# Kernel optimization log

Measured on AMD Instinct MI355X. Metric: run time of the kernel, lower is better.

## Reference

```python
import jax, jax.numpy as jnp
import numpy as np

N = 100000
E = 1600000
D_IN = 128
D_OUT = 128
NEG_SLOPE = 0.01  # PyTorch LeakyReLU default


def setup_inputs() -> dict:
    key = jax.random.key(0)
    ks = jax.random.split(key, 6)
    x = jax.random.normal(ks[0], (N, D_IN), dtype=jnp.float32)
    src = jax.random.randint(ks[1], (E,), 0, N, dtype=jnp.int32)
    dst = jax.random.randint(ks[2], (E,), 0, N, dtype=jnp.int32)
    e_attn = jax.random.uniform(ks[3], (E,), dtype=jnp.float32)
    # Xavier-normal-ish init for linear weights
    std = float(np.sqrt(2.0 / (D_IN + D_OUT)))
    W1 = jax.random.normal(ks[4], (D_OUT, D_IN), dtype=jnp.float32) * std
    W2 = jax.random.normal(ks[5], (D_OUT, D_IN), dtype=jnp.float32) * std
    b1 = jnp.zeros((D_OUT,), dtype=jnp.float32)
    b2 = jnp.zeros((D_OUT,), dtype=jnp.float32)
    return {"x": x, "src": src, "dst": dst, "e_attn": e_attn,
            "W1": W1, "b1": b1, "W2": W2, "b2": b2}


def leaky_relu(v):
    return jnp.where(v >= 0, v, NEG_SLOPE * v)


def reference(x, src, dst, e_attn, W1, b1, W2, b2):
    # Edge-weighted gather-scatter: h_n[d] = sum_{e: dst(e)=d} a_e * x[src(e)]
    msgs = x[src] * e_attn[:, None]                      # [E, D_IN]
    h_n = jax.ops.segment_sum(msgs, dst, num_segments=N)  # [N, D_IN]
    # Bi-interaction: LeakyReLU(W1(x + h_n)) + LeakyReLU(W2(x * h_n))
    add_part = leaky_relu(jnp.einsum('nd,od->no', x + h_n, W1) + b1)
    mul_part = leaky_relu(jnp.einsum('nd,od->no', x * h_n, W2) + b2)
    return add_part + mul_part  # dropout p=0.0 -> identity
```

## Files before the change

kernel.cpp:

```cpp
#include <hip/hip_runtime.h>

#define N_NODES 100000
#define E_EDGES 1600000
#define D 128
#define AP 132
#define ASTR 136

typedef short s16x8 __attribute__((ext_vector_type(8)));
typedef unsigned short u16x8 __attribute__((ext_vector_type(8)));
typedef float f32x4 __attribute__((ext_vector_type(4)));

__device__ __forceinline__ unsigned short f2bf(float f) {
    union { float f; unsigned u; } v;
    v.f = f;
    unsigned r = v.u + 0x7FFFu + ((v.u >> 16) & 1u);
    return (unsigned short)(r >> 16);
}

__device__ __forceinline__ float bf2f(unsigned short u) {
    union { unsigned u; float f; } v;
    v.u = ((unsigned)u) << 16;
    return v.f;
}

__device__ __forceinline__ float lrelu(float v) {
    return v >= 0.0f ? v : 0.01f * v;
}

__global__ __launch_bounds__(256) void prep_kernel(
    const int* __restrict__ dst, int* __restrict__ cnt,
    unsigned char* __restrict__ rank, int stride,
    const float* __restrict__ x, unsigned short* __restrict__ xbf, int do_xconv,
    const float* __restrict__ W1, const float* __restrict__ W2,
    unsigned short* __restrict__ Wswz) {
    int b = blockIdx.x;
    int t = threadIdx.x;
    if (b < 6250) {
        int e = b * 256 + t;
        rank[e] = (unsigned char)atomicAdd(&cnt[(size_t)dst[e] * stride], 1);
    } else if (b < 12500) {
        if (!do_xconv) return;
        int idx = (b - 6250) * 256 + t;
        const float4* xp = (const float4*)(x) + (size_t)idx * 2;
        float4 a = xp[0], bb = xp[1];
        u16x8 o;
        o[0] = f2bf(a.x);  o[1] = f2bf(a.y);  o[2] = f2bf(a.z);  o[3] = f2bf(a.w);
        o[4] = f2bf(bb.x); o[5] = f2bf(bb.y); o[6] = f2bf(bb.z); o[7] = f2bf(bb.w);
        ((u16x8*)(xbf))[idx] = o;
    } else {
        int tid = (b - 12500) * 256 + t;
        if (tid >= 2 * 4 * 8 * 64) return;
        int lane = tid & 63;
        int ct   = (tid >> 6) & 7;
        int ks   = (tid >> 9) & 3;
        int mat  = tid >> 11;
        const float* W = mat ? W2 : W1;
        int o  = ct * 16 + (lane & 15);
        int k0 = ks * 32 + (lane >> 4) * 8;
        const float* sp = W + (size_t)o * D + k0;
        u16x8 w;
#pragma unroll
        for (int j = 0; j < 8; ++j) w[j] = f2bf(sp[j]);
        ((u16x8*)(Wswz))[tid] = w;
    }
}

__global__ __launch_bounds__(256) void scanA_kernel(
    const int* __restrict__ cnt, int* __restrict__ excl,
    int* __restrict__ bsum, int n, int stride) {
    __shared__ int tmp[256];
    int gid = blockIdx.x * 256 + threadIdx.x;
    int v = (gid < n) ? cnt[(size_t)gid * stride] : 0;
    tmp[threadIdx.x] = v;
    __syncthreads();
    for (int ofs = 1; ofs < 256; ofs <<= 1) {
        int t = (threadIdx.x >= ofs) ? tmp[threadIdx.x - ofs] : 0;
        __syncthreads();
        tmp[threadIdx.x] += t;
        __syncthreads();
    }
    int incl = tmp[threadIdx.x];
    if (gid < n) excl[gid] = incl - v;
    if (threadIdx.x == 255) bsum[blockIdx.x] = incl;
}

__global__ __launch_bounds__(512) void scanB_kernel(int* __restrict__ bsum, int nb) {
    __shared__ int tmp[512];
    int v = (threadIdx.x < nb) ? bsum[threadIdx.x] : 0;
    tmp[threadIdx.x] = v;
    __syncthreads();
    for (int ofs = 1; ofs < 512; ofs <<= 1) {
        int t = (threadIdx.x >= ofs) ? tmp[threadIdx.x - ofs] : 0;
        __syncthreads();
        tmp[threadIdx.x] += t;
        __syncthreads();
    }
    if (threadIdx.x < nb) bsum[threadIdx.x] = tmp[threadIdx.x] - v;
}

__global__ __launch_bounds__(256) void fillC_kernel(
    const int* __restrict__ src, const int* __restrict__ dst,
    const float* __restrict__ ea, const int* __restrict__ excl,
    const int* __restrict__ bsum, const unsigned char* __restrict__ rank,
    int2* __restrict__ csr, int* __restrict__ off) {
    int gid = blockIdx.x * 256 + threadIdx.x;
    int d = dst[gid];
    int pos = excl[d] + bsum[d >> 8] + (int)rank[gid];
    csr[pos] = make_int2(src[gid], __float_as_int(ea[gid]));
    if (gid < N_NODES) off[gid] = excl[gid] + bsum[gid >> 8];
    else if (gid == N_NODES) off[N_NODES] = E_EDGES;
}

__global__ __launch_bounds__(256, 4) void fused_gg_kernel(
    const unsigned short* __restrict__ xbf, const int2* __restrict__ csr,
    const int* __restrict__ off,
    const unsigned short* __restrict__ Wswz,
    const float* __restrict__ b1, const float* __restrict__ b2,
    float* __restrict__ out) {
    __shared__ unsigned short A[2][64 * ASTR];

    const int n0 = blockIdx.x * 64;
    const int t = threadIdx.x;
    const int lane = t & 63;
    const int wv = t >> 6;
    const int q = lane >> 4;
    const int li = lane & 15;

    for (int j = 0; j < 16; ++j) {
        const int row = wv * 16 + j;
        const int node = n0 + row;
        int beg = 0, end = 0;
        if (node < N_NODES) {
            beg = off[node];
            end = off[node + 1];
        }

        float a0[8], a1[8], a2[8], a3[8];
#pragma unroll
        for (int d = 0; d < 8; ++d) { a0[d] = 0.f; a1[d] = 0.f; a2[d] = 0.f; a3[d] = 0.f; }

        int i = beg + q;
        for (; i + 12 < end; i += 16) {
            int2 p0 = csr[i];
            int2 p1 = csr[i + 4];
            int2 p2 = csr[i + 8];
            int2 p3 = csr[i + 12];
            float w0 = __int_as_float(p0.y);
            float w1 = __int_as_float(p1.y);
            float w2 = __int_as_float(p2.y);
            float w3 = __int_as_float(p3.y);
            u16x8 v0 = ((const u16x8*)(xbf + (size_t)p0.x * D))[li];
            u16x8 v1 = ((const u16x8*)(xbf + (size_t)p1.x * D))[li];
            u16x8 v2 = ((const u16x8*)(xbf + (size_t)p2.x * D))[li];
            u16x8 v3 = ((const u16x8*)(xbf + (size_t)p3.x * D))[li];
#pragma unroll
            for (int d = 0; d < 8; ++d) {
                a0[d] += w0 * bf2f(v0[d]);
                a1[d] += w1 * bf2f(v1[d]);
                a2[d] += w2 * bf2f(v2[d]);
                a3[d] += w3 * bf2f(v3[d]);
            }
        }
        for (; i < end; i += 4) {
            int2 p0 = csr[i];
            float w0 = __int_as_float(p0.y);
            u16x8 v0 = ((const u16x8*)(xbf + (size_t)p0.x * D))[li];
#pragma unroll
            for (int d = 0; d < 8; ++d) a0[d] += w0 * bf2f(v0[d]);
        }
#pragma unroll
        for (int d = 0; d < 8; ++d) a0[d] += a1[d] + a2[d] + a3[d];
#pragma unroll
        for (int d = 0; d < 8; ++d) a0[d] += __shfl_xor(a0[d], 16);
#pragma unroll
        for (int d = 0; d < 8; ++d) a0[d] += __shfl_xor(a0[d], 32);

        const int srcrow = node < N_NODES ? node : N_NODES - 1;
        if (q < 2) {
            u16x8 xu = ((const u16x8*)(xbf + (size_t)srcrow * D))[li];
            u16x8 o;
#pragma unroll
            for (int dd = 0; dd < 8; ++dd) {
                float xv = bf2f(xu[dd]);
                o[dd] = f2bf(q == 0 ? xv + a0[dd] : xv * a0[dd]);
            }
            *(u16x8*)&A[q][row * ASTR + li * 8] = o;
        }
    }

    s16x8 Bf[2][2][4];
    float bb1[2], bb2[2];
#pragma unroll
    for (int ci = 0; ci < 2; ++ci) {
        int ct = wv + ci * 4;
        bb1[ci] = b1[ct * 16 + li];
        bb2[ci] = b2[ct * 16 + li];
#pragma unroll
        for (int mat = 0; mat < 2; ++mat)
#pragma unroll
            for (int ks = 0; ks < 4; ++ks)
                Bf[ci][mat][ks] = *(const s16x8*)(
                    Wswz + ((size_t)(((mat * 4 + ks) * 8 + ct) * 64 + lane)) * 8);
    }

    __syncthreads();

    const int kq = q * 8;
#pragma unroll
    for (int mt = 0; mt < 4; ++mt) {
        f32x4 acc[2][2];
#pragma unroll
        for (int ci = 0; ci < 2; ++ci)
#pragma unroll
            for (int p = 0; p < 2; ++p) acc[ci][p] = (f32x4){0.f, 0.f, 0.f, 0.f};

        const int arow = mt * 16 + li;
#pragma unroll
        for (int ks = 0; ks < 4; ++ks) {
            s16x8 aa0 = *(const s16x8*)&A[0][arow * ASTR + ks * 32 + kq];
            s16x8 aa1 = *(const s16x8*)&A[1][arow * ASTR + ks * 32 + kq];
#pragma unroll
            for (int ci = 0; ci < 2; ++ci) {
                acc[ci][0] = __builtin_amdgcn_mfma_f32_16x16x32_bf16(
                    aa0, Bf[ci][0][ks], acc[ci][0], 0, 0, 0);
                acc[ci][1] = __builtin_amdgcn_mfma_f32_16x16x32_bf16(
                    aa1, Bf[ci][1][ks], acc[ci][1], 0, 0, 0);
            }
        }

#pragma unroll
        for (int ci = 0; ci < 2; ++ci) {
            int oc = (wv + ci * 4) * 16 + li;
#pragma unroll
            for (int r = 0; r < 4; ++r) {
                int node = n0 + mt * 16 + q * 4 + r;
                if (node < N_NODES) {
                    float v = lrelu(acc[ci][0][r] + bb1[ci])
                            + lrelu(acc[ci][1][r] + bb2[ci]);
                    out[(size_t)node * D + oc] = v;
                }
            }
        }
    }
}

__global__ __launch_bounds__(256) void gather_f32_kernel(
    const float* __restrict__ x, const int2* __restrict__ csr,
    const int* __restrict__ off, float* __restrict__ h) {
    int node = blockIdx.x * 4 + (threadIdx.x >> 6);
    int lane = threadIdx.x & 63;
    int beg = off[node];
    int end = off[node + 1];
    float2 acc0 = make_float2(0.f, 0.f);
    float2 acc1 = make_float2(0.f, 0.f);
    int e = beg;
    for (; e + 1 < end; e += 2) {
        int2 p0 = csr[e];
        int2 p1 = csr[e + 1];
        float a0 = __int_as_float(p0.y);
        float a1 = __int_as_float(p1.y);
        float2 v0 = ((const float2*)(x + (size_t)p0.x * D))[lane];
        float2 v1 = ((const float2*)(x + (size_t)p1.x * D))[lane];
        acc0.x += a0 * v0.x; acc0.y += a0 * v0.y;
        acc1.x += a1 * v1.x; acc1.y += a1 * v1.y;
    }
    if (e < end) {
        int2 p0 = csr[e];
        float a0 = __int_as_float(p0.y);
        float2 v0 = ((const float2*)(x + (size_t)p0.x * D))[lane];
        acc0.x += a0 * v0.x; acc0.y += a0 * v0.y;
    }
    acc0.x += acc1.x; acc0.y += acc1.y;
    ((float2*)(h + (size_t)node * D))[lane] = acc0;
}

__global__ __launch_bounds__(256, 4) void mfma_gemm_t1_kernel(
    const float* __restrict__ xf, const float* __restrict__ h,
    const unsigned short* __restrict__ Wswz,
    const float* __restrict__ b1, const float* __restrict__ b2,
    float* __restrict__ out) {
    __shared__ unsigned short A[2][64 * ASTR];
    const int n0 = blockIdx.x * 64;
    const int t = threadIdx.x;
    const int lane = t & 63;
    const int wv = t >> 6;
#pragma unroll
    for (int i = 0; i < 8; ++i) {
        int s = t + i * 256;
        int row = s >> 5;
        int c4 = s & 31;
        int srcrow = n0 + row;
        if (srcrow >= N_NODES) srcrow = N_NODES - 1;
        float4 xv = ((const float4*)(xf + (size_t)srcrow * D))[c4];
        float4 hv = ((const float4*)(h + (size_t)srcrow * D))[c4];
        ushort4 av, mv;
        av.x = f2bf(xv.x + hv.x); av.y = f2bf(xv.y + hv.y);
        av.z = f2bf(xv.z + hv.z); av.w = f2bf(xv.w + hv.w);
        mv.x = f2bf(xv.x * hv.x); mv.y = f2bf(xv.y * hv.y);
        mv.z = f2bf(xv.z * hv.z); mv.w = f2bf(xv.w * hv.w);
        *(ushort4*)&A[0][row * ASTR + c4 * 4] = av;
        *(ushort4*)&A[1][row * ASTR + c4 * 4] = mv;
    }
    s16x8 Bf[2][2][4];
    float bb1[2], bb2[2];
#pragma unroll
    for (int ci = 0; ci < 2; ++ci) {
        int ct = wv + ci * 4;
        bb1[ci] = b1[ct * 16 + (lane & 15)];
        bb2[ci] = b2[ct * 16 + (lane & 15)];
#pragma unroll
        for (int mat = 0; mat < 2; ++mat)
#pragma unroll
            for (int ks = 0; ks < 4; ++ks)
                Bf[ci][mat][ks] = *(const s16x8*)(
                    Wswz + ((size_t)(((mat * 4 + ks) * 8 + ct) * 64 + lane)) * 8);
    }
    __syncthreads();
    const int quad = lane >> 4;
    const int kq = quad * 8;
#pragma unroll
    for (int mt = 0; mt < 4; ++mt) {
        f32x4 acc[2][2];
#pragma unroll
        for (int ci = 0; ci < 2; ++ci)
#pragma unroll
            for (int p = 0; p < 2; ++p) acc[ci][p] = (f32x4){0.f, 0.f, 0.f, 0.f};
        const int arow = mt * 16 + (lane & 15);
#pragma unroll
        for (int ks = 0; ks < 4; ++ks) {
            s16x8 aa0 = *(const s16x8*)&A[0][arow * ASTR + ks * 32 + kq];
            s16x8 aa1 = *(const s16x8*)&A[1][arow * ASTR + ks * 32 + kq];
#pragma unroll
            for (int ci = 0; ci < 2; ++ci) {
                acc[ci][0] = __builtin_amdgcn_mfma_f32_16x16x32_bf16(
                    aa0, Bf[ci][0][ks], acc[ci][0], 0, 0, 0);
                acc[ci][1] = __builtin_amdgcn_mfma_f32_16x16x32_bf16(
                    aa1, Bf[ci][1][ks], acc[ci][1], 0, 0, 0);
            }
        }
#pragma unroll
        for (int ci = 0; ci < 2; ++ci) {
            int oc = (wv + ci * 4) * 16 + (lane & 15);
#pragma unroll
            for (int r = 0; r < 4; ++r) {
                int node = n0 + mt * 16 + quad * 4 + r;
                if (node < N_NODES) {
                    float v = lrelu(acc[ci][0][r] + bb1[ci])
                            + lrelu(acc[ci][1][r] + bb2[ci]);
                    out[(size_t)node * D + oc] = v;
                }
            }
        }
    }
}

__global__ __launch_bounds__(256) void scatter_kernel(
    const float* __restrict__ x, const int* __restrict__ src,
    const int* __restrict__ dst, const float* __restrict__ ea,
    float* __restrict__ h, int E) {
    int idx = blockIdx.x * 256 + threadIdx.x;
    int e = idx >> 5;
    int lane = idx & 31;
    if (e >= E) return;
    int s = src[e];
    int d = dst[e];
    float a = ea[e];
    float4 v = ((const float4*)(x + (size_t)s * D))[lane];
    float* hp = h + (size_t)d * D + lane * 4;
    atomicAdd(hp + 0, a * v.x);
    atomicAdd(hp + 1, a * v.y);
    atomicAdd(hp + 2, a * v.z);
    atomicAdd(hp + 3, a * v.w);
}

__global__ __launch_bounds__(256) void gemm_kernel(
    const float* __restrict__ x, const float* __restrict__ h,
    const float* __restrict__ W1, const float* __restrict__ b1,
    const float* __restrict__ W2, const float* __restrict__ b2,
    float* __restrict__ out) {
    __shared__ float Aadd[32 * AP];
    __shared__ float Amul[32 * AP];
    const int n0 = blockIdx.x * 32;
    const int t = threadIdx.x;
#pragma unroll
    for (int i = 0; i < 4; ++i) {
        int fi = t + i * 256;
        int row = fi >> 5;
        int c4 = fi & 31;
        float4 xv = ((const float4*)(x + (size_t)(n0 + row) * D))[c4];
        float4 hv = ((const float4*)(h + (size_t)(n0 + row) * D))[c4];
        float4 av = make_float4(xv.x + hv.x, xv.y + hv.y, xv.z + hv.z, xv.w + hv.w);
        float4 mv = make_float4(xv.x * hv.x, xv.y * hv.y, xv.z * hv.z, xv.w * hv.w);
        *((float4*)&Aadd[row * AP + c4 * 4]) = av;
        *((float4*)&Amul[row * AP + c4 * 4]) = mv;
    }
    __syncthreads();
    const int m0 = (t >> 5) * 4;
    const int o0 = (t & 31) * 4;
    float acc1[4][4];
    float acc2[4][4];
#pragma unroll
    for (int i = 0; i < 4; ++i)
#pragma unroll
        for (int j = 0; j < 4; ++j) { acc1[i][j] = 0.0f; acc2[i][j] = 0.0f; }
#pragma unroll 4
    for (int d = 0; d < D; d += 4) {
        float4 a[4], m[4], w1[4], w2[4];
#pragma unroll
        for (int i = 0; i < 4; ++i) a[i] = *(const float4*)&Aadd[(m0 + i) * AP + d];
#pragma unroll
        for (int i = 0; i < 4; ++i) m[i] = *(const float4*)&Amul[(m0 + i) * AP + d];
#pragma unroll
        for (int j = 0; j < 4; ++j) w1[j] = *(const float4*)&W1[(size_t)(o0 + j) * D + d];
#pragma unroll
        for (int j = 0; j < 4; ++j) w2[j] = *(const float4*)&W2[(size_t)(o0 + j) * D + d];
#pragma unroll
        for (int i = 0; i < 4; ++i)
#pragma unroll
            for (int j = 0; j < 4; ++j) {
                acc1[i][j] += a[i].x * w1[j].x + a[i].y * w1[j].y
                            + a[i].z * w1[j].z + a[i].w * w1[j].w;
                acc2[i][j] += m[i].x * w2[j].x + m[i].y * w2[j].y
                            + m[i].z * w2[j].z + m[i].w * w2[j].w;
            }
    }
#pragma unroll
    for (int i = 0; i < 4; ++i) {
        float4 r;
        float v1, v2;
        v1 = lrelu(acc1[i][0] + b1[o0 + 0]); v2 = lrelu(acc2[i][0] + b2[o0 + 0]); r.x = v1 + v2;
        v1 = lrelu(acc1[i][1] + b1[o0 + 1]); v2 = lrelu(acc2[i][1] + b2[o0 + 1]); r.y = v1 + v2;
        v1 = lrelu(acc1[i][2] + b1[o0 + 2]); v2 = lrelu(acc2[i][2] + b2[o0 + 2]); r.z = v1 + v2;
        v1 = lrelu(acc1[i][3] + b1[o0 + 3]); v2 = lrelu(acc2[i][3] + b2[o0 + 3]); r.w = v1 + v2;
        ((float4*)(out + (size_t)(n0 + m0 + i) * D))[t & 31] = r;
    }
}

extern "C" void kernel_launch(void* const* d_in, const int* in_sizes, int n_in,
                              void* d_out, int out_size, void* d_ws, size_t ws_size,
                              hipStream_t stream) {
    const float* x   = (const float*)d_in[0];
    const int*   src = (const int*)d_in[1];
    const int*   dst = (const int*)d_in[2];
    const float* ea  = (const float*)d_in[3];
    const float* W1  = (const float*)d_in[4];
    const float* b1  = (const float*)d_in[5];
    const float* W2  = (const float*)d_in[6];
    const float* b2  = (const float*)d_in[7];
    float* out = (float*)d_out;
    char* ws = (char*)d_ws;

    auto align256 = [](size_t v) { return (v + 255) & ~(size_t)255; };

    const size_t SZ_WSWZ = 2 * 4 * 8 * 64 * 8 * sizeof(unsigned short);
    const size_t SZ_OFF  = (size_t)(N_NODES + 1) * sizeof(int);
    const size_t SZ_EXCL = (size_t)N_NODES * sizeof(int);
    const size_t SZ_BSUM = 512 * sizeof(int);
    const size_t SZ_RANK = (size_t)E_EDGES;
    const size_t SZ_CSR  = (size_t)E_EDGES * sizeof(int2);
    const size_t SZ_XBF  = (size_t)N_NODES * D * sizeof(unsigned short);

    const int NB_E = 6250;
    const int NB_N = (N_NODES + 255) / 256;
    const int GB   = (N_NODES + 63) / 64;

    auto try_exact = [&](int stride) -> bool {
        size_t sz_cnt = (size_t)N_NODES * stride * sizeof(int);
        size_t o_cnt  = align256(SZ_WSWZ);
        size_t o_off  = o_cnt + align256(sz_cnt);
        size_t o_excl = o_off + align256(SZ_OFF);
        size_t o_bsum = o_excl + align256(SZ_EXCL);
        size_t o_rank = o_bsum + align256(SZ_BSUM);
        size_t o_csr  = o_rank + align256(SZ_RANK);
        size_t o_xbf  = o_csr + align256(SZ_CSR);
        size_t need   = o_xbf + align256(SZ_XBF);
        if (ws_size < need) return false;
        unsigned short* Wswz = (unsigned short*)ws;
        int*  cnt  = (int*)(ws + o_cnt);
        int*  off  = (int*)(ws + o_off);
        int*  excl = (int*)(ws + o_excl);
        int*  bsum = (int*)(ws + o_bsum);
        unsigned char* rank = (unsigned char*)(ws + o_rank);
        int2* csr  = (int2*)(ws + o_csr);
        unsigned short* xbf = (unsigned short*)(ws + o_xbf);
        hipMemsetAsync(cnt, 0, sz_cnt, stream);
        prep_kernel<<<12516, 256, 0, stream>>>(dst, cnt, rank, stride,
                                               x, xbf, 1, W1, W2, Wswz);
        scanA_kernel<<<NB_N, 256, 0, stream>>>(cnt, excl, bsum, N_NODES, stride);
        scanB_kernel<<<1, 512, 0, stream>>>(bsum, NB_N);
        fillC_kernel<<<NB_E, 256, 0, stream>>>(src, dst, ea, excl, bsum, rank,
                                               csr, off);
        fused_gg_kernel<<<GB, 256, 0, stream>>>(xbf, csr, off, Wswz, b1, b2, out);
        return true;
    };
    if (try_exact(16)) return;
    if (try_exact(1)) return;

    {
        size_t sz_cnt = (size_t)N_NODES * sizeof(int);
        size_t o_cnt  = align256(SZ_WSWZ);
        size_t o_off  = o_cnt + align256(sz_cnt);
        size_t o_excl = o_off + align256(SZ_OFF);
        size_t o_bsum = o_excl + align256(SZ_EXCL);
        size_t o_rank = o_bsum + align256(SZ_BSUM);
        size_t o_csr  = o_rank + align256(SZ_RANK);
        size_t need   = o_csr + align256(SZ_CSR);
        if (ws_size >= need) {
            unsigned short* Wswz = (unsigned short*)ws;
            int*  cnt  = (int*)(ws + o_cnt);
            int*  off  = (int*)(ws + o_off);
            int*  excl = (int*)(ws + o_excl);
            int*  bsum = (int*)(ws + o_bsum);
            unsigned char* rank = (unsigned char*)(ws + o_rank);
            int2* csr  = (int2*)(ws + o_csr);
            hipMemsetAsync(cnt, 0, sz_cnt, stream);
            prep_kernel<<<12516, 256, 0, stream>>>(dst, cnt, rank, 1,
                                                   x, nullptr, 0, W1, W2, Wswz);
            scanA_kernel<<<NB_N, 256, 0, stream>>>(cnt, excl, bsum, N_NODES, 1);
            scanB_kernel<<<1, 512, 0, stream>>>(bsum, NB_N);
            fillC_kernel<<<NB_E, 256, 0, stream>>>(src, dst, ea, excl, bsum, rank,
                                                   csr, off);
            float* h = out;
            gather_f32_kernel<<<N_NODES / 4, 256, 0, stream>>>(x, csr, off, h);
            mfma_gemm_t1_kernel<<<GB, 256, 0, stream>>>(x, h, Wswz, b1, b2, out);
            return;
        }
    }

    {
        float* h = out;
        hipMemsetAsync(h, 0, (size_t)N_NODES * D * sizeof(float), stream);
        int total = E_EDGES * 32;
        scatter_kernel<<<(total + 255) / 256, 256, 0, stream>>>(x, src, dst, ea,
                                                                h, E_EDGES);
        gemm_kernel<<<N_NODES / 32, 256, 0, stream>>>(x, h, W1, b1, W2, b2, out);
    }
}
```

Baseline: 337.6 us.

## Replace two-pass prefix scan with atomic segment allocation; widen fused block to 512

```diff
diff --git a/kernel.cpp b/kernel.cpp
--- a/kernel.cpp
+++ b/kernel.cpp
@@ -65,55 +65,39 @@
     }
 }
 
-__global__ __launch_bounds__(256) void scanA_kernel(
-    const int* __restrict__ cnt, int* __restrict__ excl,
-    int* __restrict__ bsum, int n, int stride) {
-    __shared__ int tmp[256];
+__global__ __launch_bounds__(256) void alloc_kernel(
+    const int* __restrict__ cnt, int stride, int* __restrict__ cursor,
+    int2* __restrict__ begend, int n) {
     int gid = blockIdx.x * 256 + threadIdx.x;
-    int v = (gid < n) ? cnt[(size_t)gid * stride] : 0;
-    tmp[threadIdx.x] = v;
-    __syncthreads();
-    for (int ofs = 1; ofs < 256; ofs <<= 1) {
-        int t = (threadIdx.x >= ofs) ? tmp[threadIdx.x - ofs] : 0;
-        __syncthreads();
-        tmp[threadIdx.x] += t;
-        __syncthreads();
-    }
-    int incl = tmp[threadIdx.x];
-    if (gid < n) excl[gid] = incl - v;
-    if (threadIdx.x == 255) bsum[blockIdx.x] = incl;
-}
-
-__global__ __launch_bounds__(512) void scanB_kernel(int* __restrict__ bsum, int nb) {
-    __shared__ int tmp[512];
-    int v = (threadIdx.x < nb) ? bsum[threadIdx.x] : 0;
-    tmp[threadIdx.x] = v;
-    __syncthreads();
-    for (int ofs = 1; ofs < 512; ofs <<= 1) {
-        int t = (threadIdx.x >= ofs) ? tmp[threadIdx.x - ofs] : 0;
-        __syncthreads();
-        tmp[threadIdx.x] += t;
-        __syncthreads();
-    }
-    if (threadIdx.x < nb) bsum[threadIdx.x] = tmp[threadIdx.x] - v;
+    int lane = threadIdx.x & 63;
+    int c = (gid < n) ? cnt[(size_t)gid * stride] : 0;
+    int incl = c;
+#pragma unroll
+    for (int ofs = 1; ofs < 64; ofs <<= 1) {
+        int tt = __shfl_up(incl, ofs);
+        if (lane >= ofs) incl += tt;
+    }
+    int tot = __shfl(incl, 63);
+    int base = 0;
+    if (lane == 63) base = atomicAdd(cursor, tot);
+    base = __shfl(base, 63);
+    int beg = base + incl - c;
+    if (gid < n) begend[gid] = make_int2(beg, beg + c);
 }
 
 __global__ __launch_bounds__(256) void fillC_kernel(
     const int* __restrict__ src, const int* __restrict__ dst,
-    const float* __restrict__ ea, const int* __restrict__ excl,
-    const int* __restrict__ bsum, const unsigned char* __restrict__ rank,
-    int2* __restrict__ csr, int* __restrict__ off) {
+    const float* __restrict__ ea, const int2* __restrict__ begend,
+    const unsigned char* __restrict__ rank, int2* __restrict__ csr) {
     int gid = blockIdx.x * 256 + threadIdx.x;
     int d = dst[gid];
-    int pos = excl[d] + bsum[d >> 8] + (int)rank[gid];
+    int pos = begend[d].x + (int)rank[gid];
     csr[pos] = make_int2(src[gid], __float_as_int(ea[gid]));
-    if (gid < N_NODES) off[gid] = excl[gid] + bsum[gid >> 8];
-    else if (gid == N_NODES) off[N_NODES] = E_EDGES;
-}
-
-__global__ __launch_bounds__(256, 4) void fused_gg_kernel(
+}
+
+__global__ __launch_bounds__(512, 8) void fused_gg_kernel(
     const unsigned short* __restrict__ xbf, const int2* __restrict__ csr,
-    const int* __restrict__ off,
+    const int2* __restrict__ begend,
     const unsigned short* __restrict__ Wswz,
     const float* __restrict__ b1, const float* __restrict__ b2,
     float* __restrict__ out) {
@@ -126,42 +110,35 @@
     const int q = lane >> 4;
     const int li = lane & 15;
 
-    for (int j = 0; j < 16; ++j) {
-        const int row = wv * 16 + j;
+    for (int j = 0; j < 8; ++j) {
+        const int row = wv * 8 + j;
         const int node = n0 + row;
         int beg = 0, end = 0;
         if (node < N_NODES) {
-            beg = off[node];
-            end = off[node + 1];
-        }
-
-        float a0[8], a1[8], a2[8], a3[8];
-#pragma unroll
-        for (int d = 0; d < 8; ++d) { a0[d] = 0.f; a1[d] = 0.f; a2[d] = 0.f; a3[d] = 0.f; }
+            int2 be = begend[node];
+            beg = be.x;
+            end = be.y;
+        }
+
+        float a0[8], a1[8];
+#pragma unroll
+        for (int d = 0; d < 8; ++d) { a0[d] = 0.f; a1[d] = 0.f; }
 
         int i = beg + q;
-        for (; i + 12 < end; i += 16) {
+        for (; i + 4 < end; i += 8) {
             int2 p0 = csr[i];
             int2 p1 = csr[i + 4];
-            int2 p2 = csr[i + 8];
-            int2 p3 = csr[i + 12];
             float w0 = __int_as_float(p0.y);
             float w1 = __int_as_float(p1.y);
-            float w2 = __int_as_float(p2.y);
-            float w3 = __int_as_float(p3.y);
             u16x8 v0 = ((const u16x8*)(xbf + (size_t)p0.x * D))[li];
             u16x8 v1 = ((const u16x8*)(xbf + (size_t)p1.x * D))[li];
-            u16x8 v2 = ((const u16x8*)(xbf + (size_t)p2.x * D))[li];
-            u16x8 v3 = ((const u16x8*)(xbf + (size_t)p3.x * D))[li];
 #pragma unroll
             for (int d = 0; d < 8; ++d) {
                 a0[d] += w0 * bf2f(v0[d]);
                 a1[d] += w1 * bf2f(v1[d]);
-                a2[d] += w2 * bf2f(v2[d]);
-                a3[d] += w3 * bf2f(v3[d]);
-            }
-        }
-        for (; i < end; i += 4) {
+            }
+        }
+        if (i < end) {
             int2 p0 = csr[i];
             float w0 = __int_as_float(p0.y);
             u16x8 v0 = ((const u16x8*)(xbf + (size_t)p0.x * D))[li];
@@ -169,7 +146,7 @@
             for (int d = 0; d < 8; ++d) a0[d] += w0 * bf2f(v0[d]);
         }
 #pragma unroll
-        for (int d = 0; d < 8; ++d) a0[d] += a1[d] + a2[d] + a3[d];
+        for (int d = 0; d < 8; ++d) a0[d] += a1[d];
 #pragma unroll
         for (int d = 0; d < 8; ++d) a0[d] += __shfl_xor(a0[d], 16);
 #pragma unroll
@@ -188,57 +165,41 @@
         }
     }
 
-    s16x8 Bf[2][2][4];
-    float bb1[2], bb2[2];
-#pragma unroll
-    for (int ci = 0; ci < 2; ++ci) {
-        int ct = wv + ci * 4;
-        bb1[ci] = b1[ct * 16 + li];
-        bb2[ci] = b2[ct * 16 + li];
-#pragma unroll
-        for (int mat = 0; mat < 2; ++mat)
-#pragma unroll
-            for (int ks = 0; ks < 4; ++ks)
-                Bf[ci][mat][ks] = *(const s16x8*)(
-                    Wswz + ((size_t)(((mat * 4 + ks) * 8 + ct) * 64 + lane)) * 8);
-    }
+    const int ct = wv;
+    float bb1 = b1[ct * 16 + li];
+    float bb2 = b2[ct * 16 + li];
+    s16x8 Bf[2][4];
+#pragma unroll
+    for (int mat = 0; mat < 2; ++mat)
+#pragma unroll
+        for (int ks = 0; ks < 4; ++ks)
+            Bf[mat][ks] = *(const s16x8*)(
+                Wswz + ((size_t)(((mat * 4 + ks) * 8 + ct) * 64 + lane)) * 8);
 
     __syncthreads();
 
     const int kq = q * 8;
 #pragma unroll
     for (int mt = 0; mt < 4; ++mt) {
-        f32x4 acc[2][2];
-#pragma unroll
-        for (int ci = 0; ci < 2; ++ci)
-#pragma unroll
-            for (int p = 0; p < 2; ++p) acc[ci][p] = (f32x4){0.f, 0.f, 0.f, 0.f};
+        f32x4 acc0 = (f32x4){0.f, 0.f, 0.f, 0.f};
+        f32x4 acc1 = (f32x4){0.f, 0.f, 0.f, 0.f};
 
         const int arow = mt * 16 + li;
 #pragma unroll
         for (int ks = 0; ks < 4; ++ks) {
             s16x8 aa0 = *(const s16x8*)&A[0][arow * ASTR + ks * 32 + kq];
             s16x8 aa1 = *(const s16x8*)&A[1][arow * ASTR + ks * 32 + kq];
-#pragma unroll
-            for (int ci = 0; ci < 2; ++ci) {
-                acc[ci][0] = __builtin_amdgcn_mfma_f32_16x16x32_bf16(
-                    aa0, Bf[ci][0][ks], acc[ci][0], 0, 0, 0);
-                acc[ci][1] = __builtin_amdgcn_mfma_f32_16x16x32_bf16(
-                    aa1, Bf[ci][1][ks], acc[ci][1], 0, 0, 0);
-            }
-        }
-
-#pragma unroll
-        for (int ci = 0; ci < 2; ++ci) {
-            int oc = (wv + ci * 4) * 16 + li;
-#pragma unroll
-            for (int r = 0; r < 4; ++r) {
-                int node = n0 + mt * 16 + q * 4 + r;
-                if (node < N_NODES) {
-                    float v = lrelu(acc[ci][0][r] + bb1[ci])
-                            + lrelu(acc[ci][1][r] + bb2[ci]);
-                    out[(size_t)node * D + oc] = v;
-                }
+            acc0 = __builtin_amdgcn_mfma_f32_16x16x32_bf16(aa0, Bf[0][ks], acc0, 0, 0, 0);
+            acc1 = __builtin_amdgcn_mfma_f32_16x16x32_bf16(aa1, Bf[1][ks], acc1, 0, 0, 0);
+        }
+
+        const int oc = ct * 16 + li;
+#pragma unroll
+        for (int r = 0; r < 4; ++r) {
+            int node = n0 + mt * 16 + q * 4 + r;
+            if (node < N_NODES) {
+                float v = lrelu(acc0[r] + bb1) + lrelu(acc1[r] + bb2);
+                out[(size_t)node * D + oc] = v;
             }
         }
     }
@@ -246,11 +207,12 @@
 
 __global__ __launch_bounds__(256) void gather_f32_kernel(
     const float* __restrict__ x, const int2* __restrict__ csr,
-    const int* __restrict__ off, float* __restrict__ h) {
+    const int2* __restrict__ begend, float* __restrict__ h) {
     int node = blockIdx.x * 4 + (threadIdx.x >> 6);
     int lane = threadIdx.x & 63;
-    int beg = off[node];
-    int end = off[node + 1];
+    int2 be = begend[node];
+    int beg = be.x;
+    int end = be.y;
     float2 acc0 = make_float2(0.f, 0.f);
     float2 acc1 = make_float2(0.f, 0.f);
     int e = beg;
@@ -453,9 +415,7 @@
     auto align256 = [](size_t v) { return (v + 255) & ~(size_t)255; };
 
     const size_t SZ_WSWZ = 2 * 4 * 8 * 64 * 8 * sizeof(unsigned short);
-    const size_t SZ_OFF  = (size_t)(N_NODES + 1) * sizeof(int);
-    const size_t SZ_EXCL = (size_t)N_NODES * sizeof(int);
-    const size_t SZ_BSUM = 512 * sizeof(int);
+    const size_t SZ_BE   = (size_t)N_NODES * sizeof(int2);
     const size_t SZ_RANK = (size_t)E_EDGES;
     const size_t SZ_CSR  = (size_t)E_EDGES * sizeof(int2);
     const size_t SZ_XBF  = (size_t)N_NODES * D * sizeof(unsigned short);
@@ -464,64 +424,56 @@
     const int NB_N = (N_NODES + 255) / 256;
     const int GB   = (N_NODES + 63) / 64;
 
-    auto try_exact = [&](int stride) -> bool {
+    auto try_top = [&](int stride) -> bool {
         size_t sz_cnt = (size_t)N_NODES * stride * sizeof(int);
         size_t o_cnt  = align256(SZ_WSWZ);
-        size_t o_off  = o_cnt + align256(sz_cnt);
-        size_t o_excl = o_off + align256(SZ_OFF);
-        size_t o_bsum = o_excl + align256(SZ_EXCL);
-        size_t o_rank = o_bsum + align256(SZ_BSUM);
+        size_t o_cur  = o_cnt + align256(sz_cnt);
+        size_t o_be   = o_cur + 256;
+        size_t o_rank = o_be + align256(SZ_BE);
         size_t o_csr  = o_rank + align256(SZ_RANK);
         size_t o_xbf  = o_csr + align256(SZ_CSR);
         size_t need   = o_xbf + align256(SZ_XBF);
         if (ws_size < need) return false;
         unsigned short* Wswz = (unsigned short*)ws;
         int*  cnt  = (int*)(ws + o_cnt);
-        int*  off  = (int*)(ws + o_off);
-        int*  excl = (int*)(ws + o_excl);
-        int*  bsum = (int*)(ws + o_bsum);
+        int*  cur  = (int*)(ws + o_cur);
+        int2* be   = (int2*)(ws + o_be);
         unsigned char* rank = (unsigned char*)(ws + o_rank);
         int2* csr  = (int2*)(ws + o_csr);
         unsigned short* xbf = (unsigned short*)(ws + o_xbf);
-        hipMemsetAsync(cnt, 0, sz_cnt, stream);
+        hipMemsetAsync(cnt, 0, align256(sz_cnt) + 256, stream);
         prep_kernel<<<12516, 256, 0, stream>>>(dst, cnt, rank, stride,
                                                x, xbf, 1, W1, W2, Wswz);
-        scanA_kernel<<<NB_N, 256, 0, stream>>>(cnt, excl, bsum, N_NODES, stride);
-        scanB_kernel<<<1, 512, 0, stream>>>(bsum, NB_N);
-        fillC_kernel<<<NB_E, 256, 0, stream>>>(src, dst, ea, excl, bsum, rank,
-                                               csr, off);
-        fused_gg_kernel<<<GB, 256, 0, stream>>>(xbf, csr, off, Wswz, b1, b2, out);
+        alloc_kernel<<<NB_N, 256, 0, stream>>>(cnt, stride, cur, be, N_NODES);
+        fillC_kernel<<<NB_E, 256, 0, stream>>>(src, dst, ea, be, rank, csr);
+        fused_gg_kernel<<<GB, 512, 0, stream>>>(xbf, csr, be, Wswz, b1, b2, out);
         return true;
     };
-    if (try_exact(16)) return;
-    if (try_exact(1)) return;
+    if (try_top(16)) return;
+    if (try_top(1)) return;
 
     {
         size_t sz_cnt = (size_t)N_NODES * sizeof(int);
         size_t o_cnt  = align256(SZ_WSWZ);
-        size_t o_off  = o_cnt + align256(sz_cnt);
-        size_t o_excl = o_off + align256(SZ_OFF);
-        size_t o_bsum = o_excl + align256(SZ_EXCL);
-        size_t o_rank = o_bsum + align256(SZ_BSUM);
+        size_t o_cur  = o_cnt + align256(sz_cnt);
+        size_t o_be   = o_cur + 256;
+        size_t o_rank = o_be + align256(SZ_BE);
         size_t o_csr  = o_rank + align256(SZ_RANK);
         size_t need   = o_csr + align256(SZ_CSR);
         if (ws_size >= need) {
             unsigned short* Wswz = (unsigned short*)ws;
             int*  cnt  = (int*)(ws + o_cnt);
-            int*  off  = (int*)(ws + o_off);
-            int*  excl = (int*)(ws + o_excl);
-            int*  bsum = (int*)(ws + o_bsum);
+            int*  cur  = (int*)(ws + o_cur);
+            int2* be   = (int2*)(ws + o_be);
             unsigned char* rank = (unsigned char*)(ws + o_rank);
             int2* csr  = (int2*)(ws + o_csr);
-            hipMemsetAsync(cnt, 0, sz_cnt, stream);
+            hipMemsetAsync(cnt, 0, align256(sz_cnt) + 256, stream);
             prep_kernel<<<12516, 256, 0, stream>>>(dst, cnt, rank, 1,
                                                    x, nullptr, 0, W1, W2, Wswz);
-            scanA_kernel<<<NB_N, 256, 0, stream>>>(cnt, excl, bsum, N_NODES, 1);
-            scanB_kernel<<<1, 512, 0, stream>>>(bsum, NB_N);
-            fillC_kernel<<<NB_E, 256, 0, stream>>>(src, dst, ea, excl, bsum, rank,
-                                                   csr, off);
+            alloc_kernel<<<NB_N, 256, 0, stream>>>(cnt, 1, cur, be, N_NODES);
+            fillC_kernel<<<NB_E, 256, 0, stream>>>(src, dst, ea, be, rank, csr);
             float* h = out;
-            gather_f32_kernel<<<N_NODES / 4, 256, 0, stream>>>(x, csr, off, h);
+            gather_f32_kernel<<<N_NODES / 4, 256, 0, stream>>>(x, csr, be, h);
             mfma_gemm_t1_kernel<<<GB, 256, 0, stream>>>(x, h, Wswz, b1, b2, out);
             return;
         }
```

Result: faster. 319.6 us (-5.3%).
